# Optimization experiments

Hardware: AMD Instinct MI355X
Metric: run time of the kernel (lower is better)

Reference implementation:

```python
import jax, jax.numpy as jnp
import numpy as np

N_NODES = 50000
N_EDGES = 800000
D_FEAT = 64


def setup_inputs() -> dict:
    key = jax.random.key(0)
    k1, k2, k3, k4 = jax.random.split(key, 4)
    row_idx = jnp.sort(jax.random.randint(k1, (N_EDGES,), 0, N_NODES, dtype=jnp.int32))
    col_idx = jax.random.randint(k2, (N_EDGES,), 0, N_NODES, dtype=jnp.int32)
    vals = jax.random.uniform(k3, (N_EDGES,), dtype=jnp.float32)
    embeds = jax.random.normal(k4, (N_NODES, D_FEAT), dtype=jnp.float32)
    return {"row_idx": row_idx, "col_idx": col_idx, "vals": vals, "embeds": embeds}


def reference(row_idx, col_idx, vals, embeds):
    # SpMM: out[r] = sum_{e: row[e]==r} vals[e] * embeds[col[e]]
    gathered = vals[:, None] * embeds[col_idx]          # [E, D]
    out = jax.ops.segment_sum(gathered, row_idx, num_segments=N_NODES)  # [N, D]
    return out
```

## Files before the change

### kernel.cpp

```cpp
#include <hip/hip_runtime.h>
#include <hip/hip_fp16.h>


constexpr int N_NODES = 50000;
constexpr int N_EDGES = 800000;
constexpr int D_FEAT  = 64;

using half4 = __attribute__((ext_vector_type(4))) _Float16;
using half8 = __attribute__((ext_vector_type(8))) _Float16;

constexpr size_t WS_ROWPTR_OFF = 0;
constexpr size_t WS_TBL0_OFF   = 4u << 20;
constexpr size_t WS_TBL1_OFF   = 8u << 20;

constexpr int ROWPTR_BLOCKS  = (N_EDGES + 255) / 256;
constexpr int CONVERT_BLOCKS = (N_NODES * 16 + 255) / 256;

__global__ __launch_bounds__(256) void prep_kernel(
    const int*   __restrict__ row_idx,
    const float* __restrict__ embeds,
    int*         __restrict__ row_ptr,
    _Float16*    __restrict__ tbl0,
    _Float16*    __restrict__ tbl1)
{
    if (blockIdx.x < ROWPTR_BLOCKS) {
        const int e = blockIdx.x * 256 + threadIdx.x;
        if (e >= N_EDGES) return;
        const int r     = row_idx[e];
        const int rprev = (e == 0) ? -1 : row_idx[e - 1];
        for (int q = rprev + 1; q <= r; ++q) row_ptr[q] = e;
        if (e == N_EDGES - 1) {
            for (int q = r + 1; q <= N_NODES; ++q) row_ptr[q] = N_EDGES;
        }
    } else {
        const int t = (blockIdx.x - ROWPTR_BLOCKS) * 256 + threadIdx.x;
        if (t >= N_NODES * 16) return;
        const int r = t >> 4;
        const int k = t & 15;
        const float4 v = ((const float4*)embeds)[t];
        half4 hv;
        hv[0] = (_Float16)v.x; hv[1] = (_Float16)v.y;
        hv[2] = (_Float16)v.z; hv[3] = (_Float16)v.w;
        _Float16* tbl = (k < 8) ? tbl0 : tbl1;
        ((half4*)tbl)[r * 8 + (k & 7)] = hv;
    }
}

__global__ __launch_bounds__(256) void gcn_spmm_kernel(
    const int*      __restrict__ row_ptr,
    const int*      __restrict__ col_idx,
    const float*    __restrict__ vals,
    const _Float16* __restrict__ tbl0,
    const _Float16* __restrict__ tbl1,
    float*          __restrict__ out)
{
    const int s   = blockIdx.x & 1;
    const int row = (blockIdx.x >> 1) * 4 + (threadIdx.x >> 6);
    if (row >= N_NODES) return;

    const int lane = threadIdx.x & 63;
    const int g    = lane >> 2;
    const int h    = lane & 3;

    const int es = row_ptr[row];
    const int ee = row_ptr[row + 1];

    const half8* __restrict__ tbl8 =
        (const half8*)(s ? tbl1 : tbl0);

    float acc[8] = {0.f, 0.f, 0.f, 0.f, 0.f, 0.f, 0.f, 0.f};

    for (int base = es; base < ee; base += 16) {
        const int   edge = base + g;
        const int   ce   = (edge < ee) ? edge : (ee - 1);
        const int   c    = col_idx[ce];
        const float v    = (edge < ee) ? vals[ce] : 0.f;
        const half8 gv   = tbl8[c * 4 + h];
#pragma unroll
        for (int i = 0; i < 8; ++i) acc[i] += v * (float)gv[i];
    }

#pragma unroll
    for (int mask = 4; mask <= 32; mask <<= 1) {
#pragma unroll
        for (int i = 0; i < 8; ++i) acc[i] += __shfl_xor(acc[i], mask);
    }

    if (g == 0) {
        float4* o4 = (float4*)out;
        o4[row * 16 + s * 8 + h * 2 + 0] =
            make_float4(acc[0], acc[1], acc[2], acc[3]);
        o4[row * 16 + s * 8 + h * 2 + 1] =
            make_float4(acc[4], acc[5], acc[6], acc[7]);
    }
}

extern "C" void kernel_launch(void* const* d_in, const int* in_sizes, int n_in,
                              void* d_out, int out_size, void* d_ws, size_t ws_size,
                              hipStream_t stream) {
    const int*   row_idx = (const int*)  d_in[0];
    const int*   col_idx = (const int*)  d_in[1];
    const float* vals    = (const float*)d_in[2];
    const float* embeds  = (const float*)d_in[3];
    float*       out     = (float*)      d_out;

    char* ws = (char*)d_ws;
    int*      row_ptr = (int*)     (ws + WS_ROWPTR_OFF);
    _Float16* tbl0    = (_Float16*)(ws + WS_TBL0_OFF);
    _Float16* tbl1    = (_Float16*)(ws + WS_TBL1_OFF);

    prep_kernel<<<ROWPTR_BLOCKS + CONVERT_BLOCKS, 256, 0, stream>>>(
        row_idx, embeds, row_ptr, tbl0, tbl1);

    gcn_spmm_kernel<<<25000, 256, 0, stream>>>(row_ptr, col_idx, vals,
                                               tbl0, tbl1, out);
}
```

Measured before the change: 111.7 us.

## Merge split fp16 tables into one row-major table, one wave per full row

Replaces the two half-width fp16 embedding tables, which were each processed by a separate block per row, with a single contiguous fp16 table. Each wave now covers all 64 features of a row, with 8 lanes per edge and two edges per iteration. This halves the number of col_idx/vals/row_ptr reads and blocks, and gathers a full 128-byte row per edge. Nontemporal loads and stores are added for streamed data. The trade-off is fewer independent blocks in flight and more registers per thread for the two-edge unroll.

```diff
diff --git a/kernel.cpp b/kernel.cpp
--- a/kernel.cpp
+++ b/kernel.cpp
@@ -8,10 +8,10 @@
 
 using half4 = __attribute__((ext_vector_type(4))) _Float16;
 using half8 = __attribute__((ext_vector_type(8))) _Float16;
+using fvec4 = __attribute__((ext_vector_type(4))) float;
 
 constexpr size_t WS_ROWPTR_OFF = 0;
-constexpr size_t WS_TBL0_OFF   = 4u << 20;
-constexpr size_t WS_TBL1_OFF   = 8u << 20;
+constexpr size_t WS_TBL_OFF    = 1u << 20;
 
 constexpr int ROWPTR_BLOCKS  = (N_EDGES + 255) / 256;
 constexpr int CONVERT_BLOCKS = (N_NODES * 16 + 255) / 256;
@@ -20,8 +20,7 @@
     const int*   __restrict__ row_idx,
     const float* __restrict__ embeds,
     int*         __restrict__ row_ptr,
-    _Float16*    __restrict__ tbl0,
-    _Float16*    __restrict__ tbl1)
+    _Float16*    __restrict__ tbl)
 {
     if (blockIdx.x < ROWPTR_BLOCKS) {
         const int e = blockIdx.x * 256 + threadIdx.x;
@@ -35,14 +34,11 @@
     } else {
         const int t = (blockIdx.x - ROWPTR_BLOCKS) * 256 + threadIdx.x;
         if (t >= N_NODES * 16) return;
-        const int r = t >> 4;
-        const int k = t & 15;
-        const float4 v = ((const float4*)embeds)[t];
+        const fvec4 v = __builtin_nontemporal_load(((const fvec4*)embeds) + t);
         half4 hv;
         hv[0] = (_Float16)v.x; hv[1] = (_Float16)v.y;
         hv[2] = (_Float16)v.z; hv[3] = (_Float16)v.w;
-        _Float16* tbl = (k < 8) ? tbl0 : tbl1;
-        ((half4*)tbl)[r * 8 + (k & 7)] = hv;
+        ((half4*)tbl)[t] = hv;
     }
 }
 
@@ -50,48 +46,54 @@
     const int*      __restrict__ row_ptr,
     const int*      __restrict__ col_idx,
     const float*    __restrict__ vals,
-    const _Float16* __restrict__ tbl0,
-    const _Float16* __restrict__ tbl1,
+    const _Float16* __restrict__ tbl,
     float*          __restrict__ out)
 {
-    const int s   = blockIdx.x & 1;
-    const int row = (blockIdx.x >> 1) * 4 + (threadIdx.x >> 6);
+    const int row = blockIdx.x * 4 + (threadIdx.x >> 6);
     if (row >= N_NODES) return;
 
     const int lane = threadIdx.x & 63;
-    const int g    = lane >> 2;
-    const int h    = lane & 3;
+    const int g    = lane >> 3;
+    const int h    = lane & 7;
 
     const int es = row_ptr[row];
     const int ee = row_ptr[row + 1];
 
-    const half8* __restrict__ tbl8 =
-        (const half8*)(s ? tbl1 : tbl0);
+    const half8* __restrict__ tbl8 = (const half8*)tbl;
 
     float acc[8] = {0.f, 0.f, 0.f, 0.f, 0.f, 0.f, 0.f, 0.f};
 
     for (int base = es; base < ee; base += 16) {
-        const int   edge = base + g;
-        const int   ce   = (edge < ee) ? edge : (ee - 1);
-        const int   c    = col_idx[ce];
-        const float v    = (edge < ee) ? vals[ce] : 0.f;
-        const half8 gv   = tbl8[c * 4 + h];
+        const int e0 = base + g;
+        const int e1 = base + 8 + g;
+        const int c0i = (e0 < ee) ? e0 : (ee - 1);
+        const int c1i = (e1 < ee) ? e1 : (ee - 1);
+        const int   c0 = __builtin_nontemporal_load(col_idx + c0i);
+        const int   c1 = __builtin_nontemporal_load(col_idx + c1i);
+        const float v0 = (e0 < ee) ? __builtin_nontemporal_load(vals + c0i) : 0.f;
+        const float v1 = (e1 < ee) ? __builtin_nontemporal_load(vals + c1i) : 0.f;
+        const half8 g0 = tbl8[c0 * 8 + h];
+        const half8 g1 = tbl8[c1 * 8 + h];
 #pragma unroll
-        for (int i = 0; i < 8; ++i) acc[i] += v * (float)gv[i];
+        for (int i = 0; i < 8; ++i) {
+            acc[i] += v0 * (float)g0[i];
+            acc[i] += v1 * (float)g1[i];
+        }
     }
 
 #pragma unroll
-    for (int mask = 4; mask <= 32; mask <<= 1) {
+    for (int mask = 8; mask <= 32; mask <<= 1) {
 #pragma unroll
         for (int i = 0; i < 8; ++i) acc[i] += __shfl_xor(acc[i], mask);
     }
 
     if (g == 0) {
-        float4* o4 = (float4*)out;
-        o4[row * 16 + s * 8 + h * 2 + 0] =
-            make_float4(acc[0], acc[1], acc[2], acc[3]);
-        o4[row * 16 + s * 8 + h * 2 + 1] =
-            make_float4(acc[4], acc[5], acc[6], acc[7]);
+        fvec4* o4 = (fvec4*)(out + row * D_FEAT + h * 8);
+        fvec4 lo, hi;
+        lo.x = acc[0]; lo.y = acc[1]; lo.z = acc[2]; lo.w = acc[3];
+        hi.x = acc[4]; hi.y = acc[5]; hi.z = acc[6]; hi.w = acc[7];
+        __builtin_nontemporal_store(lo, o4);
+        __builtin_nontemporal_store(hi, o4 + 1);
     }
 }
 
@@ -106,12 +108,11 @@
 
     char* ws = (char*)d_ws;
     int*      row_ptr = (int*)     (ws + WS_ROWPTR_OFF);
-    _Float16* tbl0    = (_Float16*)(ws + WS_TBL0_OFF);
-    _Float16* tbl1    = (_Float16*)(ws + WS_TBL1_OFF);
+    _Float16* tbl     = (_Float16*)(ws + WS_TBL_OFF);
 
     prep_kernel<<<ROWPTR_BLOCKS + CONVERT_BLOCKS, 256, 0, stream>>>(
-        row_idx, embeds, row_ptr, tbl0, tbl1);
+        row_idx, embeds, row_ptr, tbl);
 
-    gcn_spmm_kernel<<<25000, 256, 0, stream>>>(row_ptr, col_idx, vals,
-                                               tbl0, tbl1, out);
+    gcn_spmm_kernel<<<(N_NODES + 3) / 4, 256, 0, stream>>>(
+        row_ptr, col_idx, vals, tbl, out);
 }
```

After: 99.93 us. 1.12x faster.
